# Optimization experiments

Measured on AMD Instinct MI355X. Metric: run time of the kernel, lower is better.

## Reference

```python
import jax, jax.numpy as jnp
import numpy as np

IN_F = 4096
OUT_F = 4096
B, S = 4, 2048


def _quantize_weight(w_float):
    """Replicates Int4PackedLinear.__init__ double quantization; returns reg_b and w_scale."""
    w_amax = jnp.abs(w_float).max()
    scale = jnp.where(w_amax == 0, 1.0, w_amax / 127.0)
    w_int8 = jnp.clip(jnp.round(w_float / scale), -127, 127).astype(jnp.int8)
    low4_amax = jnp.abs(w_int8.astype(jnp.float32)).max()
    low4_scale = jnp.where(low4_amax == 0, 1.0, low4_amax / 7.0)
    w_low = jnp.clip(jnp.round(w_int8.astype(jnp.float32) / low4_scale), -7, 7).astype(jnp.int8)
    w_rec = jnp.round(w_low.astype(jnp.float32) * low4_scale).astype(jnp.int8)
    w_high = jnp.clip(w_int8.astype(jnp.int32) - w_rec.astype(jnp.int32), -7, 7).astype(jnp.int8)
    reg_b = (w_rec.astype(jnp.int32) + w_high.astype(jnp.int32)).astype(jnp.int8)  # w_combined
    return reg_b, scale.astype(jnp.float32)


def setup_inputs() -> dict:
    key = jax.random.key(0)
    k1, k2, k3 = jax.random.split(key, 3)
    w_float = jax.random.normal(k1, (OUT_F, IN_F), dtype=jnp.float32) * 0.02
    reg_b, w_scale = _quantize_weight(w_float)
    x = jax.random.normal(k2, (B, S, IN_F), dtype=jnp.float32)
    bias = jax.random.normal(k3, (OUT_F,), dtype=jnp.float32) * 0.01
    # gate=1.0 >= threshold=0.3 -> full-precision INT8 path uses reg_b
    return {"x": x, "w_int": reg_b, "w_scale": w_scale, "bias": bias}


def reference(x, w_int, w_scale, bias):
    # --- dynamic per-tensor activation quantization ---
    x_amax = jnp.abs(x).max()
    x_scale = jnp.where(x_amax == 0, jnp.float32(1.0), x_amax / 127.0)
    x_int8 = jnp.clip(jnp.round(x / x_scale), -127, 127).astype(jnp.int8)
    # --- integer matmul (accumulate in int32, like torch._int_mm) ---
    out_i32 = jnp.einsum(
        'bsk,nk->bsn',
        x_int8.astype(jnp.int32),
        w_int.astype(jnp.int32),
    )  # [B, S, OUT_F]
    # --- dequant scale in bf16 AFTER the integer matmul, then bias add ---
    combined_scale = (x_scale * w_scale).astype(jnp.bfloat16)
    out = out_i32.astype(jnp.bfloat16) * combined_scale
    out = out + bias  # bf16 + fp32 -> fp32, matching torch promotion
    return out
```

## Files before the change

### kernel.cpp

```cpp
#include <hip/hip_runtime.h>
#include <hip/hip_bf16.h>
#include <stdint.h>

#define IN_F  4096
#define OUT_F 4096
#define BSZ   4
#define SEQ   2048
#define MDIM  (BSZ * SEQ)

typedef __attribute__((address_space(1))) uint8_t ga_u8_t;
typedef __attribute__((address_space(3))) uint8_t ls_u8_t;

__device__ __forceinline__ void gload16_lds(const void* g, void* l) {
    __builtin_amdgcn_global_load_lds((ga_u8_t*)g, (ls_u8_t*)l, 16, 0, 0);
}

__device__ __forceinline__ float bf16_rne(float f) {
    unsigned u = __float_as_uint(f);
    u = (u + 0x7fffu + ((u >> 16) & 1u)) & 0xffff0000u;
    return __uint_as_float(u);
}

__global__ void amax_kernel(const float* __restrict__ x, int n4,
                            unsigned int* __restrict__ amax_u) {
    const float4* x4 = (const float4*)x;
    int idx = blockIdx.x * blockDim.x + threadIdx.x;
    int stride = gridDim.x * blockDim.x;
    float m = 0.0f;
    for (int i = idx; i < n4; i += stride) {
        float4 v = x4[i];
        m = fmaxf(m, fmaxf(fmaxf(fabsf(v.x), fabsf(v.y)),
                           fmaxf(fabsf(v.z), fabsf(v.w))));
    }
    for (int off = 32; off > 0; off >>= 1)
        m = fmaxf(m, __shfl_down(m, off, 64));
    __shared__ float sm[4];
    int lane = threadIdx.x & 63, wave = threadIdx.x >> 6;
    if (lane == 0) sm[wave] = m;
    __syncthreads();
    if (threadIdx.x == 0) {
        m = fmaxf(fmaxf(sm[0], sm[1]), fmaxf(sm[2], sm[3]));
        atomicMax(amax_u, __float_as_uint(m));
    }
}

__global__ void quant_kernel(const float* __restrict__ x,
                             signed char* __restrict__ x8,
                             const unsigned int* __restrict__ amax_u, int n4) {
    float amax = __uint_as_float(*amax_u);
    float xs = (amax == 0.0f) ? 1.0f : (amax / 127.0f);
    int idx = blockIdx.x * blockDim.x + threadIdx.x;
    if (idx < n4) {
        float4 v = ((const float4*)x)[idx];
        char4 q;
        q.x = (signed char)fminf(fmaxf(rintf(v.x / xs), -127.0f), 127.0f);
        q.y = (signed char)fminf(fmaxf(rintf(v.y / xs), -127.0f), 127.0f);
        q.z = (signed char)fminf(fmaxf(rintf(v.z / xs), -127.0f), 127.0f);
        q.w = (signed char)fminf(fmaxf(rintf(v.w / xs), -127.0f), 127.0f);
        ((char4*)x8)[idx] = q;
    }
}

__global__ void convw_kernel(const int* __restrict__ w,
                             signed char* __restrict__ w8, int n4) {
    int idx = blockIdx.x * blockDim.x + threadIdx.x;
    if (idx < n4) {
        int4 v = ((const int4*)w)[idx];
        char4 q;
        q.x = (signed char)v.x; q.y = (signed char)v.y;
        q.z = (signed char)v.z; q.w = (signed char)v.w;
        ((char4*)w8)[idx] = q;
    }
}

__global__ __launch_bounds__(256, 2) void gemm_i8_kernel(
    const signed char* __restrict__ A,
    const signed char* __restrict__ B,
    const unsigned int* __restrict__ amax_u,
    const float* __restrict__ wscale_p,
    const float* __restrict__ bias,
    float* __restrict__ out) {
    __shared__ signed char sA[128 * 64];
    __shared__ signed char sB[128 * 64];

    const int t = threadIdx.x;
    const int lane = t & 63;
    const int wave = t >> 6;
    const int wm = wave >> 1;
    const int wn = wave & 1;
    const int tileM = blockIdx.y * 128;
    const int tileN = blockIdx.x * 128;

    const int g0 = t, g1 = t + 256;
    const int ar0 = g0 >> 2, ac0 = ((g0 & 3) ^ ((ar0 >> 1) & 3)) * 16;
    const int ar1 = g1 >> 2, ac1 = ((g1 & 3) ^ ((ar1 >> 1) & 3)) * 16;

    const signed char* gA0 = A + (size_t)(tileM + ar0) * IN_F + ac0;
    const signed char* gA1 = A + (size_t)(tileM + ar1) * IN_F + ac1;
    const signed char* gB0 = B + (size_t)(tileN + ar0) * IN_F + ac0;
    const signed char* gB1 = B + (size_t)(tileN + ar1) * IN_F + ac1;

    signed char* lA0 = sA + g0 * 16;
    signed char* lA1 = sA + g1 * 16;
    signed char* lB0 = sB + g0 * 16;
    signed char* lB1 = sB + g1 * 16;

    using i32x4 = __attribute__((ext_vector_type(4))) int;
    i32x4 acc[4][4] = {};

    const signed char* aptr[4];
    const signed char* bptr[4];
#pragma unroll
    for (int i = 0; i < 4; ++i) {
        int rowa = wm * 64 + i * 16 + (lane & 15);
        int ca = ((lane >> 4) ^ ((rowa >> 1) & 3)) * 16;
        aptr[i] = sA + rowa * 64 + ca;
        int rowb = wn * 64 + i * 16 + (lane & 15);
        int cb = ((lane >> 4) ^ ((rowb >> 1) & 3)) * 16;
        bptr[i] = sB + rowb * 64 + cb;
    }

    for (int k0 = 0; k0 < IN_F; k0 += 64) {
        __syncthreads();
        gload16_lds(gA0 + k0, lA0);
        gload16_lds(gA1 + k0, lA1);
        gload16_lds(gB0 + k0, lB0);
        gload16_lds(gB1 + k0, lB1);
        __syncthreads();

        i32x4 aF[4], bF[4];
#pragma unroll
        for (int i = 0; i < 4; ++i) aF[i] = *(const i32x4*)aptr[i];
#pragma unroll
        for (int j = 0; j < 4; ++j) bF[j] = *(const i32x4*)bptr[j];
#pragma unroll
        for (int i = 0; i < 4; ++i)
#pragma unroll
            for (int j = 0; j < 4; ++j)
                acc[i][j] = __builtin_amdgcn_mfma_i32_16x16x64_i8(
                    aF[i], bF[j], acc[i][j], 0, 0, 0);
    }

    float amax = __uint_as_float(*amax_u);
    float xs = (amax == 0.0f) ? 1.0f : (amax / 127.0f);
    float cs = bf16_rne(xs * wscale_p[0]);

#pragma unroll
    for (int j = 0; j < 4; ++j) {
        int n = tileN + wn * 64 + j * 16 + (lane & 15);
        float bz = bias[n];
#pragma unroll
        for (int i = 0; i < 4; ++i) {
            int row0 = tileM + wm * 64 + i * 16 + (lane >> 4) * 4;
#pragma unroll
            for (int r = 0; r < 4; ++r) {
                float v = bf16_rne((float)acc[i][j][r]);
                float p = bf16_rne(v * cs);
                out[(size_t)(row0 + r) * OUT_F + n] = p + bz;
            }
        }
    }
}

extern "C" void kernel_launch(void* const* d_in, const int* in_sizes, int n_in,
                              void* d_out, int out_size, void* d_ws,
                              size_t ws_size, hipStream_t stream) {
    const float* x = (const float*)d_in[0];
    const int* w_int = (const int*)d_in[1];
    const float* w_scale = (const float*)d_in[2];
    const float* bias = (const float*)d_in[3];
    float* out = (float*)d_out;

    unsigned char* ws = (unsigned char*)d_ws;
    unsigned int* amax_u = (unsigned int*)ws;
    signed char* w8 = (signed char*)(ws + 64);
    signed char* x8 = (signed char*)(ws + 64 + (size_t)OUT_F * IN_F);

    hipMemsetAsync(amax_u, 0, 4, stream);

    const int n_x = MDIM * IN_F;
    const int n_w = OUT_F * IN_F;

    amax_kernel<<<4096, 256, 0, stream>>>(x, n_x / 4, amax_u);
    quant_kernel<<<(n_x / 4) / 256, 256, 0, stream>>>(x, x8, amax_u, n_x / 4);
    convw_kernel<<<(n_w / 4) / 256, 256, 0, stream>>>(w_int, w8, n_w / 4);

    dim3 grid(OUT_F / 128, MDIM / 128);
    gemm_i8_kernel<<<grid, 256, 0, stream>>>(x8, w8, amax_u, w_scale, bias, out);
}
```

Before: 472.6 us.

## Fuse quant and weight conversion, swizzle GEMM tile order, use nontemporal stores

Merges the activation quantization and weight int32-to-int8 conversion into one kernel launch, which removes a launch and lets the two memory-bound passes share the machine. The GEMM now uses a 1D grid with a grouped tile mapping (8 M-tiles per group across all 32 N-tiles), so concurrently running blocks share A and B rows in L2. Output stores become nontemporal so the large fp32 result does not evict cached operands.

```diff
diff --git a/kernel.cpp b/kernel.cpp
--- a/kernel.cpp
+++ b/kernel.cpp
@@ -44,13 +44,16 @@
     }
 }
 
-__global__ void quant_kernel(const float* __restrict__ x,
-                             signed char* __restrict__ x8,
-                             const unsigned int* __restrict__ amax_u, int n4) {
-    float amax = __uint_as_float(*amax_u);
-    float xs = (amax == 0.0f) ? 1.0f : (amax / 127.0f);
+__global__ void prep_kernel(const float* __restrict__ x,
+                            const int* __restrict__ w,
+                            signed char* __restrict__ x8,
+                            signed char* __restrict__ w8,
+                            const unsigned int* __restrict__ amax_u,
+                            int nx4, int nw4) {
     int idx = blockIdx.x * blockDim.x + threadIdx.x;
-    if (idx < n4) {
+    if (idx < nx4) {
+        float amax = __uint_as_float(*amax_u);
+        float xs = (amax == 0.0f) ? 1.0f : (amax / 127.0f);
         float4 v = ((const float4*)x)[idx];
         char4 q;
         q.x = (signed char)fminf(fmaxf(rintf(v.x / xs), -127.0f), 127.0f);
@@ -58,20 +61,19 @@
         q.z = (signed char)fminf(fmaxf(rintf(v.z / xs), -127.0f), 127.0f);
         q.w = (signed char)fminf(fmaxf(rintf(v.w / xs), -127.0f), 127.0f);
         ((char4*)x8)[idx] = q;
+    } else {
+        int widx = idx - nx4;
+        if (widx < nw4) {
+            int4 v = ((const int4*)w)[widx];
+            char4 q;
+            q.x = (signed char)v.x; q.y = (signed char)v.y;
+            q.z = (signed char)v.z; q.w = (signed char)v.w;
+            ((char4*)w8)[widx] = q;
+        }
     }
 }
 
-__global__ void convw_kernel(const int* __restrict__ w,
-                             signed char* __restrict__ w8, int n4) {
-    int idx = blockIdx.x * blockDim.x + threadIdx.x;
-    if (idx < n4) {
-        int4 v = ((const int4*)w)[idx];
-        char4 q;
-        q.x = (signed char)v.x; q.y = (signed char)v.y;
-        q.z = (signed char)v.z; q.w = (signed char)v.w;
-        ((char4*)w8)[idx] = q;
-    }
-}
+using i32x4 = __attribute__((ext_vector_type(4))) int;
 
 __global__ __launch_bounds__(256, 2) void gemm_i8_kernel(
     const signed char* __restrict__ A,
@@ -88,8 +90,12 @@
     const int wave = t >> 6;
     const int wm = wave >> 1;
     const int wn = wave & 1;
-    const int tileM = blockIdx.y * 128;
-    const int tileN = blockIdx.x * 128;
+
+    const int bid = blockIdx.x;
+    const int mt = (bid >> 8) * 8 + (bid & 7);
+    const int nt = (bid & 255) >> 3;
+    const int tileM = mt * 128;
+    const int tileN = nt * 128;
 
     const int g0 = t, g1 = t + 256;
     const int ar0 = g0 >> 2, ac0 = ((g0 & 3) ^ ((ar0 >> 1) & 3)) * 16;
@@ -105,7 +111,6 @@
     signed char* lB0 = sB + g0 * 16;
     signed char* lB1 = sB + g1 * 16;
 
-    using i32x4 = __attribute__((ext_vector_type(4))) int;
     i32x4 acc[4][4] = {};
 
     const signed char* aptr[4];
@@ -156,7 +161,8 @@
             for (int r = 0; r < 4; ++r) {
                 float v = bf16_rne((float)acc[i][j][r]);
                 float p = bf16_rne(v * cs);
-                out[(size_t)(row0 + r) * OUT_F + n] = p + bz;
+                __builtin_nontemporal_store(
+                    p + bz, &out[(size_t)(row0 + r) * OUT_F + n]);
             }
         }
     }
@@ -178,13 +184,14 @@
 
     hipMemsetAsync(amax_u, 0, 4, stream);
 
-    const int n_x = MDIM * IN_F;
-    const int n_w = OUT_F * IN_F;
+    const int n_x4 = MDIM * IN_F / 4;
+    const int n_w4 = OUT_F * IN_F / 4;
 
-    amax_kernel<<<4096, 256, 0, stream>>>(x, n_x / 4, amax_u);
-    quant_kernel<<<(n_x / 4) / 256, 256, 0, stream>>>(x, x8, amax_u, n_x / 4);
-    convw_kernel<<<(n_w / 4) / 256, 256, 0, stream>>>(w_int, w8, n_w / 4);
+    amax_kernel<<<4096, 256, 0, stream>>>(x, n_x4, amax_u);
+    prep_kernel<<<(n_x4 + n_w4) / 256, 256, 0, stream>>>(
+        x, w_int, x8, w8, amax_u, n_x4, n_w4);
 
-    dim3 grid(OUT_F / 128, MDIM / 128);
-    gemm_i8_kernel<<<grid, 256, 0, stream>>>(x8, w8, amax_u, w_scale, bias, out);
+    const int nblocks = (MDIM / 128) * (OUT_F / 128);
+    gemm_i8_kernel<<<nblocks, 256, 0, stream>>>(x8, w8, amax_u, w_scale, bias,
+                                                out);
 }
```

After: 459.3 us. 2.8% less time.
